# Optimization experiments

Hardware: AMD Instinct MI355X
Metric: run time of the kernel (lower is better)

The kernel has to match this reference:

```python
import jax, jax.numpy as jnp
import numpy as np

T = 4096; D = 768; V = 32000; L = 4; EPS = 1e-5


def _ln(x, g, b):
    m = jnp.mean(x, axis=-1, keepdims=True)
    v = jnp.mean((x - m) ** 2, axis=-1, keepdims=True)
    return (x - m) * jax.lax.rsqrt(v + EPS) * g + b


def _qgelu(x):
    return x * jax.nn.sigmoid(1.702 * x)


def setup_inputs() -> dict:
    key = jax.random.key(0)
    ks = jax.random.split(key, 10)
    s = 0.02
    return {
        "idx": jax.random.randint(ks[0], (T,), 0, V),
        "wte": jax.random.normal(ks[1], (V, D)) * s,
        "rb_ln_g": jnp.ones((D,)), "rb_ln_b": jnp.zeros((D,)),
        "rb_fc_w": jax.random.normal(ks[2], (D, 4 * D)) * s,
        "rb_fc_b": jnp.zeros((4 * D,)),
        "rb_proj_w": jax.random.normal(ks[3], (4 * D, D)) * s,
        "rb_proj_b": jnp.zeros((D,)),
        "lnf_g": jnp.ones((D,)), "lnf_b": jnp.zeros((D,)),
        "lm_head_w": jax.random.normal(ks[4], (D, V)) * s,
        "mb_ln_g": jnp.ones((L, 2 * D)), "mb_ln_b": jnp.zeros((L, 2 * D)),
        "mb_fc_w": jax.random.normal(ks[5], (L, 2 * D, 4 * D)) * s,
        "mb_fc_b": jnp.zeros((L, 4 * D)),
        "mb_proj_w": jax.random.normal(ks[6], (L, 4 * D, D)) * s,
        "mb_proj_b": jnp.zeros((L, D)),
        "op_w": jax.random.normal(ks[7], (L, D, D)) * s,
        "op_b": jnp.zeros((L, D)),
        "lns_g": jnp.ones((L, D)), "lns_b": jnp.zeros((L, D)),
        "heads_w": jax.random.normal(ks[8], (L, D, V)) * s,
    }


def reference(idx, wte, rb_ln_g, rb_ln_b, rb_fc_w, rb_fc_b, rb_proj_w, rb_proj_b,
              lnf_g, lnf_b, lm_head_w, mb_ln_g, mb_ln_b, mb_fc_w, mb_fc_b,
              mb_proj_w, mb_proj_b, op_w, op_b, lns_g, lns_b, heads_w):
    # token embedding (dropout is identity in eval) + initial residual block
    x = wte[idx]  # [T, D]
    h = _ln(x, rb_ln_g, rb_ln_b)
    x = x + _qgelu(h @ rb_fc_w + rb_fc_b) @ rb_proj_w + rb_proj_b
    x = _ln(x, lnf_g, lnf_b)
    logits = x @ lm_head_w  # [T, V]

    # targets=None path: pred_targets = cat(idx[1:], [-1])
    pred_targets = jnp.concatenate([idx[1:], jnp.full((1,), -1, idx.dtype)])
    pos = jnp.arange(T)
    skey = jax.random.key(42)

    for i in range(L):  # static small loop over layers
        j = i + 1
        # multinomial(softmax(logits), 1) == categorical(logits)
        idx_next = jax.random.categorical(jax.random.fold_in(skey, i), logits)
        # positions p where the sample matched the next-token target and p < T - j
        mask = (idx_next == pred_targets) & (pos < T - j)  # [T] bool
        # x2[p] = x[p + j] (padded); compute merge densely, select with mask
        x2 = jnp.concatenate([x[j:], jnp.zeros((j, D), x.dtype)], axis=0)
        h = _ln(jnp.concatenate([x, x2], axis=-1), mb_ln_g[i], mb_ln_b[i])
        merged = x2 + _qgelu(h @ mb_fc_w[i] + mb_fc_b[i]) @ mb_proj_w[i] + mb_proj_b[i]
        # scatter merged[p] into x at position p + j where mask[p]
        merged_s = jnp.concatenate([jnp.zeros((j, D), x.dtype), merged[:-j]], axis=0)
        mask_s = jnp.concatenate([jnp.zeros((j,), bool), mask[:-j]], axis=0)
        x = jnp.where(mask_s[:, None], merged_s, x)
        x = x @ op_w[i] + op_b[i]
        x = _ln(x, lns_g[i], lns_b[i])
        logits = x @ heads_w[i]
    return logits
```

## Files before the change

kernel.cpp:

```cpp
#include <hip/hip_runtime.h>
#include <cstdint>
#include <cstddef>

#define T_TOK 4096
#define DIM   768
#define VOCAB 32000
#define NLAYER 4
#define HALF_TV 65536000u

typedef short bf16x8 __attribute__((ext_vector_type(8)));
typedef float f32x4  __attribute__((ext_vector_type(4)));
typedef float f32x4v __attribute__((ext_vector_type(4)));

__host__ __device__ inline void tf2x32(uint32_t k0, uint32_t k1, uint32_t& v0, uint32_t& v1){
  uint32_t ks2 = k0 ^ k1 ^ 0x1BD11BDAu;
  uint32_t x0 = v0 + k0, x1 = v1 + k1;
#define TFR(R) { x0 += x1; x1 = (x1<<R)|(x1>>(32-R)); x1 ^= x0; }
  TFR(13) TFR(15) TFR(26) TFR(6)
  x0 += k1;  x1 += ks2 + 1u;
  TFR(17) TFR(29) TFR(16) TFR(24)
  x0 += ks2; x1 += k0 + 2u;
  TFR(13) TFR(15) TFR(26) TFR(6)
  x0 += k0;  x1 += k1 + 3u;
  TFR(17) TFR(29) TFR(16) TFR(24)
  x0 += k1;  x1 += ks2 + 4u;
  TFR(13) TFR(15) TFR(26) TFR(6)
  x0 += ks2; x1 += k0 + 5u;
#undef TFR
  v0 = x0; v1 = x1;
}

__device__ inline float neglog_u(uint32_t k){
  float L;
  if (k >= 0x780000u){
    float x = (float)(0x800000u - k) * 1.1920928955078125e-7f;
    L = x * fmaf(x, fmaf(x, fmaf(x, 0.25f, 0.3333333333333f), 0.5f), 1.0f);
  } else {
    float l2k = __builtin_amdgcn_logf((float)k);
    L = 0.69314718055994531f * (23.0f - l2k);
    if (k == 0u) L = 87.33654475055310898f;
  }
  return L;
}

__device__ inline void gumbel_pair(uint32_t kf0, uint32_t kf1, uint32_t t_up, uint32_t v,
                                   float& gu, float& gd){
  uint32_t m = t_up * (uint32_t)VOCAB + v;
  uint32_t x0 = m, x1 = m + HALF_TV;
  tf2x32(kf0, kf1, x0, x1);
  float Lu = neglog_u(x0 >> 9);
  float Ld = neglog_u(x1 >> 9);
  gu = -0.69314718055994531f * __builtin_amdgcn_logf(Lu);
  gd = -0.69314718055994531f * __builtin_amdgcn_logf(Ld);
}

__device__ inline unsigned short f2bf(float f){
  uint32_t u = __float_as_uint(f);
  return (unsigned short)((u + 0x7FFFu + ((u >> 16) & 1u)) >> 16);
}
__device__ inline float bf2f(unsigned short h){
  return __uint_as_float(((uint32_t)h) << 16);
}
__device__ inline void cvt8(const float* f, bool lo, unsigned short* out){
  #pragma unroll
  for (int e=0;e<8;e++){
    float x = f[e];
    unsigned short h = f2bf(x);
    if (lo) h = f2bf(x - bf2f(h));
    out[e] = h;
  }
}
__device__ inline float blockReduceSum(float v){
  __shared__ float red[4];
  #pragma unroll
  for (int off=32; off>0; off>>=1) v += __shfl_down(v, off);
  int w = threadIdx.x >> 6;
  __syncthreads();
  if ((threadIdx.x & 63) == 0) red[w] = v;
  __syncthreads();
  return red[0] + red[1] + red[2] + red[3];
}

__device__ inline void gload16(const void* g, void* l){
  __builtin_amdgcn_global_load_lds(
      (const __attribute__((address_space(1))) unsigned int*)g,
      (__attribute__((address_space(3))) unsigned int*)l, 16, 0, 0);
}

enum { ST_F32 = 0, ST_HILO = 1, ST_SAMPLE = 2 };

template<int KSTEPS, int NSEG, int STORE, bool NTST, bool BIAS, bool QGELU>
__global__ __launch_bounds__(1024, 4) void k_hgemm256(
    const unsigned short* __restrict__ A0, const unsigned short* __restrict__ A1,
    const unsigned short* __restrict__ B0, const unsigned short* __restrict__ B2,
    float* __restrict__ C, unsigned short* __restrict__ Ch, unsigned short* __restrict__ Cl,
    const float* __restrict__ bias, uint32_t kf0, uint32_t kf1,
    unsigned long long* __restrict__ row_best, int N)
{
  constexpr int K  = KSTEPS * 64;
  constexpr int NT = NSEG * KSTEPS;
  __shared__ unsigned short sAll[65536];

  const int t = threadIdx.x;
  const int w = t >> 6, l = t & 63;
  const int wm = w >> 2, wn = w & 3;
  const int g = l >> 4, r = l & 15;

  int bid = blockIdx.x;
  int xcd = bid & 7, c = bid >> 3;
  int bm = xcd*2 + (c & 1);
  int bn = c >> 1;

  f32x4 acc[4][4] = {};

  size_t arow[2], brow[2];
  #pragma unroll
  for (int p=0;p<2;p++){
    int mr = p*128 + (t >> 3);
    int blk = mr >> 4;
    arow[p] = (size_t)(bm*128 + ((blk>>1)<<4) + (mr & 15) + ((blk & 1) ? 2048 : 0)) * K;
    int nr = p*128 + (t >> 3);
    brow[p] = (size_t)(bn*256 + nr) * K;
  }
  const int swz  = ((t & 7) ^ ((t >> 3) & 7)) << 3;
  const int ldst = t * 16;

  auto stage = [&](int vt){
    char* base = (char*)sAll + (vt & 1) * 65536;
    int seg = (NSEG == 1) ? 0 : (vt / KSTEPS);
    int k0  = ((NSEG == 1) ? vt : (vt % KSTEPS)) * 64;
    const unsigned short* Ap = (seg == 1) ? A1 : A0;
    const unsigned short* Bp = (seg == 2) ? B2 : B0;
    #pragma unroll
    for (int p=0;p<2;p++)
      gload16(Ap + arow[p] + k0 + swz, base + p*16384 + ldst);
    #pragma unroll
    for (int p=0;p<2;p++)
      gload16(Bp + brow[p] + k0 + swz, base + 32768 + p*16384 + ldst);
  };

  stage(0);
  __syncthreads();

  for (int vt = 0; vt < NT; ++vt){
    if (vt + 1 < NT) stage(vt + 1);
    const char* sA = (const char*)sAll + (vt & 1) * 65536;
    const char* sB = sA + 32768;
    #pragma unroll
    for (int kk=0;kk<2;kk++){
      bf16x8 bv[4], av[4];
      #pragma unroll
      for (int ni=0;ni<4;ni++){
        int tr = wn*64 + ni*16 + r;
        bv[ni] = *(const bf16x8*)(sB + tr*128 + (((kk*4+g) ^ (r&7))<<4));
      }
      #pragma unroll
      for (int q=0;q<4;q++){
        int tr = wm*64 + q*16 + r;
        av[q] = *(const bf16x8*)(sA + tr*128 + (((kk*4+g) ^ (r&7))<<4));
      }
      __builtin_amdgcn_s_setprio(1);
      #pragma unroll
      for (int q=0;q<4;q++)
        #pragma unroll
        for (int ni=0;ni<4;ni++)
          acc[q][ni] = __builtin_amdgcn_mfma_f32_16x16x32_bf16(av[q], bv[ni], acc[q][ni], 0, 0, 0);
      __builtin_amdgcn_s_setprio(0);
    }
    __syncthreads();
  }

  if constexpr (STORE == ST_SAMPLE){
    #pragma unroll
    for (int mi=0; mi<4; mi+=2){
      int row16 = (wm*2 + (mi>>1)) * 16;
      #pragma unroll
      for (int jj=0;jj<4;jj++){
        uint32_t t_up = bm*128 + row16 + g*4 + jj;
        unsigned long long bu = 0ull, bd = 0ull;
        #pragma unroll
        for (int ni=0;ni<4;ni++){
          uint32_t v = bn*256 + wn*64 + ni*16 + r;
          float gu, gd;
          gumbel_pair(kf0, kf1, t_up, v, gu, gd);
          float vu = acc[mi][ni][jj]   + gu;
          float vd = acc[mi+1][ni][jj] + gd;
          uint32_t fu = __float_as_uint(vu); fu = (fu & 0x80000000u) ? ~fu : (fu | 0x80000000u);
          uint32_t fd = __float_as_uint(vd); fd = (fd & 0x80000000u) ? ~fd : (fd | 0x80000000u);
          unsigned long long pu = ((unsigned long long)fu << 32) | (unsigned long long)(~v);
          unsigned long long pd = ((unsigned long long)fd << 32) | (unsigned long long)(~v);
          if (pu > bu) bu = pu;
          if (pd > bd) bd = pd;
        }
        #pragma unroll
        for (int off=1; off<16; off<<=1){
          unsigned int l0 = (unsigned int)bu, h0 = (unsigned int)(bu>>32);
          unsigned int l1 = __shfl_xor(l0, off), h1 = __shfl_xor(h0, off);
          unsigned long long o = ((unsigned long long)h1 << 32) | (unsigned long long)l1;
          if (o > bu) bu = o;
          l0 = (unsigned int)bd; h0 = (unsigned int)(bd>>32);
          l1 = __shfl_xor(l0, off); h1 = __shfl_xor(h0, off);
          o = ((unsigned long long)h1 << 32) | (unsigned long long)l1;
          if (o > bd) bd = o;
        }
        if (r == 0){
          atomicMax(&row_best[t_up], bu);
          atomicMax(&row_best[t_up + 2048], bd);
        }
      }
    }
  } else {
    #pragma unroll
    for (int mi=0;mi<4;mi++){
      int blk = wm*4 + mi;
      int mbase = bm*128 + ((blk>>1)<<4) + ((blk & 1) ? 2048 : 0);
      #pragma unroll
      for (int ni=0;ni<4;ni++){
        int n = bn*256 + wn*64 + ni*16 + r;
        float bv_ = BIAS ? bias[n] : 0.0f;
        #pragma unroll
        for (int jj=0;jj<4;jj++){
          int m = mbase + g*4 + jj;
          float v = acc[mi][ni][jj] + bv_;
          if constexpr (QGELU) v = v / (1.0f + expf(-1.702f * v));
          if constexpr (STORE == ST_F32){
            if constexpr (NTST) __builtin_nontemporal_store(v, &C[(size_t)m * N + n]);
            else                C[(size_t)m * N + n] = v;
          } else {
            unsigned short h = f2bf(v);
            Ch[(size_t)m * N + n] = h;
            Cl[(size_t)m * N + n] = f2bf(v - bf2f(h));
          }
        }
      }
    }
  }
}

template<int KSTEPS, int NSEG, bool BIAS, bool QGELU, bool RES, int STORE>
__global__ __launch_bounds__(256) void k_hgemm(
    const unsigned short* __restrict__ A0, const unsigned short* __restrict__ A1,
    const unsigned short* __restrict__ B0, const unsigned short* __restrict__ B2,
    float* __restrict__ C, unsigned short* __restrict__ Ch, unsigned short* __restrict__ Cl,
    const float* __restrict__ bias, const float* __restrict__ res,
    int N, uint32_t kf0, uint32_t kf1, unsigned long long* __restrict__ row_best)
{
  constexpr int K = KSTEPS * 64;
  __shared__ unsigned short sA[128*64];
  __shared__ unsigned short sB[128*64];
  const int t = threadIdx.x;
  const int wave = t >> 6, lane = t & 63;
  const int wm = wave >> 1, wn = wave & 1;
  const int g = lane >> 4, r = lane & 15;
  const int lr = lane >> 3, lc = lane & 7;

  int bid = blockIdx.x;
  int xcd = bid & 7, c = bid >> 3;
  int bm = xcd*4 + (c & 3);
  int bn = c >> 2;

  f32x4 acc[4][4] = {};

  for (int kb = 0; kb < NSEG*KSTEPS; ++kb){
    const int seg = (NSEG == 1) ? 0 : (kb / KSTEPS);
    const int k0  = (NSEG == 1) ? kb*64 : (kb % KSTEPS) * 64;
    const unsigned short* Ap = (seg == 1) ? A1 : A0;
    const unsigned short* Bp = (seg == 2) ? B2 : B0;
    __syncthreads();
    #pragma unroll
    for (int p=0;p<4;p++){
      int mr = p*32 + wave*8 + lr;
      int blk = mr >> 4;
      int grow = bm*64 + ((blk>>1)<<4) + (mr & 15) + ((blk & 1) ? 2048 : 0);
      int gk = k0 + ((lc ^ lr) << 3);
      gload16(Ap + (size_t)grow * K + gk, (char*)sA + mr*128 + lc*16);
      int nrow = bn*128 + mr;
      gload16(Bp + (size_t)nrow * K + gk, (char*)sB + mr*128 + lc*16);
    }
    __syncthreads();
    #pragma unroll
    for (int kk=0;kk<2;kk++){
      bf16x8 av[4], bv[4];
      #pragma unroll
      for (int mi=0;mi<4;mi++){
        int tr = wm*64 + mi*16 + r;
        av[mi] = *(const bf16x8*)((const char*)sA + tr*128 + (((kk*4+g) ^ (r&7))<<4));
      }
      #pragma unroll
      for (int ni=0;ni<4;ni++){
        int tr = wn*64 + ni*16 + r;
        bv[ni] = *(const bf16x8*)((const char*)sB + tr*128 + (((kk*4+g) ^ (r&7))<<4));
      }
      #pragma unroll
      for (int mi=0;mi<4;mi++)
        #pragma unroll
        for (int ni=0;ni<4;ni++)
          acc[mi][ni] = __builtin_amdgcn_mfma_f32_16x16x32_bf16(av[mi], bv[ni], acc[mi][ni], 0, 0, 0);
    }
  }

  #pragma unroll
  for (int mi=0;mi<4;mi++){
    int blk2 = wm*4 + mi;
    int mbase = bm*64 + ((blk2>>1)<<4) + ((blk2 & 1) ? 2048 : 0);
    #pragma unroll
    for (int ni=0;ni<4;ni++){
      int n = bn*128 + wn*64 + ni*16 + r;
      float bv_ = BIAS ? bias[n] : 0.0f;
      #pragma unroll
      for (int jj=0;jj<4;jj++){
        int m = mbase + g*4 + jj;
        float v = acc[mi][ni][jj] + bv_;
        if constexpr (QGELU) v = v / (1.0f + expf(-1.702f * v));
        if constexpr (RES)   v += res[(size_t)m * N + n];
        if constexpr (STORE == ST_F32){
          C[(size_t)m * N + n] = v;
        } else {
          unsigned short h = f2bf(v);
          Ch[(size_t)m * N + n] = h;
          Cl[(size_t)m * N + n] = f2bf(v - bf2f(h));
        }
      }
    }
  }
}

template<bool SPLIT>
__global__ __launch_bounds__(256) void k_wt_t(const float* __restrict__ W,
    unsigned short* __restrict__ Bh, unsigned short* __restrict__ Bl, int K, int N)
{
  __shared__ unsigned short sH[64][72];
  __shared__ unsigned short sL[64][72];
  int kt = blockIdx.x, nt = blockIdx.y;
  int t = threadIdx.x;
  int kr = t >> 4, nc4 = (t & 15) * 4;
  #pragma unroll
  for (int p=0;p<4;p++){
    int k = p*16 + kr;
    f32x4v w = __builtin_nontemporal_load((const f32x4v*)&W[(size_t)(kt*64 + k) * N + nt*64 + nc4]);
    #pragma unroll
    for (int e=0;e<4;e++){
      unsigned short h = f2bf(w[e]);
      sH[nc4+e][k] = h;
      if (SPLIT) sL[nc4+e][k] = f2bf(w[e] - bf2f(h));
    }
  }
  __syncthreads();
  #pragma unroll
  for (int q=0;q<2;q++){
    int cid = t + q*256;
    int n = cid >> 3, ch = cid & 7;
    *(bf16x8*)&Bh[(size_t)(nt*64+n)*K + kt*64 + ch*8] = *(const bf16x8*)&sH[n][ch*8];
    if (SPLIT)
      *(bf16x8*)&Bl[(size_t)(nt*64+n)*K + kt*64 + ch*8] = *(const bf16x8*)&sL[n][ch*8];
  }
}

__global__ __launch_bounds__(256) void k_embed_ln(const int* __restrict__ idx,
    const float* __restrict__ wte, const float* __restrict__ g, const float* __restrict__ b,
    float* __restrict__ Xraw, unsigned short* __restrict__ Hh, unsigned short* __restrict__ Hl)
{
  int row = blockIdx.x;
  const float* src = wte + (size_t)idx[row] * DIM;
  float v[3];
  #pragma unroll
  for (int jj=0;jj<3;jj++) v[jj] = src[threadIdx.x + jj*256];
  float s = blockReduceSum(v[0]+v[1]+v[2]);
  float mean = s * (1.0f/DIM);
  float s2 = 0;
  #pragma unroll
  for (int jj=0;jj<3;jj++){ float d = v[jj]-mean; s2 += d*d; }
  s2 = blockReduceSum(s2);
  float rs = rsqrtf(s2 * (1.0f/DIM) + 1e-5f);
  #pragma unroll
  for (int jj=0;jj<3;jj++){
    int d = threadIdx.x + jj*256;
    Xraw[(size_t)row*DIM + d] = v[jj];
    float o = (v[jj]-mean)*rs*g[d] + b[d];
    unsigned short h = f2bf(o);
    Hh[(size_t)row*DIM + d] = h;
    Hl[(size_t)row*DIM + d] = f2bf(o - bf2f(h));
  }
}

__global__ __launch_bounds__(256) void k_ln(const float* __restrict__ in, float* __restrict__ out,
    const float* __restrict__ g, const float* __restrict__ b,
    unsigned short* __restrict__ obf, unsigned short* __restrict__ olo)
{
  int row = blockIdx.x;
  const float* src = in + (size_t)row * DIM;
  float v[3];
  #pragma unroll
  for (int jj=0;jj<3;jj++) v[jj] = src[threadIdx.x + jj*256];
  float s = blockReduceSum(v[0]+v[1]+v[2]);
  float mean = s * (1.0f/DIM);
  float s2 = 0;
  #pragma unroll
  for (int jj=0;jj<3;jj++){ float d = v[jj]-mean; s2 += d*d; }
  s2 = blockReduceSum(s2);
  float rs = rsqrtf(s2 * (1.0f/DIM) + 1e-5f);
  #pragma unroll
  for (int jj=0;jj<3;jj++){
    int d = threadIdx.x + jj*256;
    float o = (v[jj]-mean)*rs*g[d] + b[d];
    out[(size_t)row*DIM + d] = o;
    unsigned short h = f2bf(o);
    obf[(size_t)row*DIM + d] = h;
    olo[(size_t)row*DIM + d] = f2bf(o - bf2f(h));
  }
}

__global__ void k_mask(const unsigned long long* __restrict__ row_best,
    const int* __restrict__ idx, int j, int* __restrict__ count, int* __restrict__ plist)
{
  int t = blockIdx.x * blockDim.x + threadIdx.x;
  if (t >= T_TOK) return;
  int v = (int)(~(uint32_t)(row_best[t] & 0xFFFFFFFFull));
  int tgt = (t < T_TOK-1) ? idx[t+1] : -1;
  if (v == tgt && t < T_TOK - j){
    int pos = atomicAdd(count, 1);
    plist[pos] = t;
  }
}

__global__ __launch_bounds__(256) void k_merge(const float* __restrict__ X,
    const int* __restrict__ plist, const int* __restrict__ count,
    const float* __restrict__ lng, const float* __restrict__ lnb,
    const float* __restrict__ fcw, const float* __restrict__ fcb,
    const float* __restrict__ pjw, const float* __restrict__ pjb,
    float* __restrict__ mergebuf, int j)
{
  __shared__ float sh[1536 + 3072];
  int nb = *count;
  for (int bIdx = blockIdx.x; bIdx < nb; bIdx += gridDim.x){
    int p = plist[bIdx];
    const float* xp = X + (size_t)p * DIM;
    const float* x2 = X + (size_t)(p + j) * DIM;
    for (int d = threadIdx.x; d < 1536; d += 256)
      sh[d] = (d < DIM) ? xp[d] : x2[d - DIM];
    __syncthreads();
    float s = 0;
    for (int d = threadIdx.x; d < 1536; d += 256) s += sh[d];
    s = blockReduceSum(s);
    float mean = s * (1.0f/1536.0f);
    float s2 = 0;
    for (int d = threadIdx.x; d < 1536; d += 256){ float df = sh[d]-mean; s2 += df*df; }
    s2 = blockReduceSum(s2);
    float rs = rsqrtf(s2 * (1.0f/1536.0f) + 1e-5f);
    __syncthreads();
    for (int d = threadIdx.x; d < 1536; d += 256)
      sh[d] = (sh[d]-mean)*rs*lng[d] + lnb[d];
    __syncthreads();
    float* act = sh + 1536;
    #pragma unroll
    for (int jj=0;jj<12;jj++){
      int n = threadIdx.x + jj*256;
      float a = fcb[n];
      for (int k=0;k<1536;k++) a += sh[k]*fcw[(size_t)k*3072 + n];
      act[n] = a / (1.0f + expf(-1.702f*a));
    }
    __syncthreads();
    #pragma unroll
    for (int jj=0;jj<3;jj++){
      int d = threadIdx.x + jj*256;
      float a = pjb[d];
      for (int k=0;k<3072;k++) a += act[k]*pjw[(size_t)k*DIM + d];
      mergebuf[(size_t)bIdx*DIM + d] = x2[d] + a;
    }
    __syncthreads();
  }
}

__global__ void k_scatter(float* __restrict__ X, unsigned short* __restrict__ Xbf,
    unsigned short* __restrict__ Xlo, const float* __restrict__ mergebuf,
    const int* __restrict__ plist, const int* __restrict__ count, int j)
{
  int nb = *count;
  for (int bIdx = blockIdx.x; bIdx < nb; bIdx += gridDim.x){
    int p = plist[bIdx];
    for (int d = threadIdx.x; d < DIM; d += 256){
      float v = mergebuf[(size_t)bIdx*DIM + d];
      size_t o = (size_t)(p + j)*DIM + d;
      X[o] = v;
      unsigned short h = f2bf(v);
      Xbf[o] = h;
      Xlo[o] = f2bf(v - bf2f(h));
    }
  }
}

__global__ __launch_bounds__(256) void k_gemm_old(
    const float* __restrict__ A, const float* __restrict__ B, float* __restrict__ C,
    int M, int N, int K)
{
  __shared__ unsigned short sA[128*64];
  __shared__ unsigned short sB[128*64];
  const int t = threadIdx.x;
  const int bn = blockIdx.x, bm = blockIdx.y;
  const int wave = t >> 6, lane = t & 63;
  const int wm = wave >> 1, wn = wave & 1;
  const int g = lane >> 4, r = lane & 15;
  f32x4 acc[4][4] = {};
  const int nK = K >> 6;
  const int aC = t & 7,  aM0 = t >> 3;
  const int bN0 = t & 31, bC = t >> 5;
  const float* Abase = A + (size_t)(bm*128) * K;
  const float* Bbase = B + (size_t)(bn*128);
  for (int seg = 0; seg < 3; ++seg) {
    const bool aLO = (seg == 1), bLO = (seg == 2);
    for (int kb = 0; kb < nK; ++kb) {
      const int k0 = kb << 6;
      __syncthreads();
      #pragma unroll
      for (int p=0;p<4;p++){
        int m = p*32 + aM0;
        const float* src = Abase + (size_t)m * K + k0 + aC*8;
        float ff[8];
        *(float4*)(ff)   = *(const float4*)(src);
        *(float4*)(ff+4) = *(const float4*)(src+4);
        unsigned short hh[8];
        cvt8(ff, aLO, hh);
        *(bf16x8*)&sA[m*64 + ((aC ^ (m & 7)) * 8)] = *(bf16x8*)hh;
      }
      #pragma unroll
      for (int p=0;p<4;p++){
        int n = p*32 + bN0;
        float ff[8];
        const float* src = Bbase + (size_t)(k0 + bC*8) * N + n;
        #pragma unroll
        for (int e=0;e<8;e++) ff[e] = src[(size_t)e * N];
        unsigned short hh[8];
        cvt8(ff, bLO, hh);
        *(bf16x8*)&sB[n*64 + ((bC ^ (n & 7)) * 8)] = *(bf16x8*)hh;
      }
      __syncthreads();
      #pragma unroll
      for (int kk=0;kk<2;kk++){
        bf16x8 av[4], bv[4];
        #pragma unroll
        for (int mi=0;mi<4;mi++){
          int m = wm*64 + mi*16 + r;
          av[mi] = *(const bf16x8*)&sA[m*64 + (((kk*4 + g) ^ (m & 7)) * 8)];
        }
        #pragma unroll
        for (int ni=0;ni<4;ni++){
          int n = wn*64 + ni*16 + r;
          bv[ni] = *(const bf16x8*)&sB[n*64 + (((kk*4 + g) ^ (n & 7)) * 8)];
        }
        #pragma unroll
        for (int mi=0;mi<4;mi++)
          #pragma unroll
          for (int ni=0;ni<4;ni++)
            acc[mi][ni] = __builtin_amdgcn_mfma_f32_16x16x32_bf16(av[mi], bv[ni], acc[mi][ni], 0, 0, 0);
      }
    }
  }
  #pragma unroll
  for (int mi=0;mi<4;mi++)
    #pragma unroll
    for (int ni=0;ni<4;ni++)
      #pragma unroll
      for (int jj=0;jj<4;jj++){
        int m = bm*128 + wm*64 + mi*16 + g*4 + jj;
        int n = bn*128 + wn*64 + ni*16 + r;
        C[(size_t)m * N + n] = acc[mi][ni][jj];
      }
}

static void fold_key(uint32_t i, uint32_t& o0, uint32_t& o1){
  uint32_t x0 = 0, x1 = i;
  tf2x32(0u, 42u, x0, x1);
  o0 = x0; o1 = x1;
}

extern "C" void kernel_launch(void* const* d_in, const int* in_sizes, int n_in,
                              void* d_out, int out_size, void* d_ws, size_t ws_size,
                              hipStream_t stream)
{
  const int*   idx       = (const int*)  d_in[0];
  const float* wte       = (const float*)d_in[1];
  const float* rb_ln_g   = (const float*)d_in[2];
  const float* rb_ln_b   = (const float*)d_in[3];
  const float* rb_fc_w   = (const float*)d_in[4];
  const float* rb_fc_b   = (const float*)d_in[5];
  const float* rb_proj_w = (const float*)d_in[6];
  const float* rb_proj_b = (const float*)d_in[7];
  const float* lnf_g     = (const float*)d_in[8];
  const float* lnf_b     = (const float*)d_in[9];
  const float* lm_head_w = (const float*)d_in[10];
  const float* mb_ln_g   = (const float*)d_in[11];
  const float* mb_ln_b   = (const float*)d_in[12];
  const float* mb_fc_w   = (const float*)d_in[13];
  const float* mb_fc_b   = (const float*)d_in[14];
  const float* mb_proj_w = (const float*)d_in[15];
  const float* mb_proj_b = (const float*)d_in[16];
  const float* op_w      = (const float*)d_in[17];
  const float* op_b      = (const float*)d_in[18];
  const float* lns_g     = (const float*)d_in[19];
  const float* lns_b     = (const float*)d_in[20];
  const float* heads_w   = (const float*)d_in[21];

  const size_t TD = (size_t)T_TOK * DIM;
  const size_t DV = (size_t)DIM * VOCAB;

  float* X = (float*)d_ws;
  float* Y = X + TD;
  unsigned short* Xbf = (unsigned short*)(Y + TD);
  unsigned short* Xlo = Xbf + TD;
  unsigned short* BtFh = Xlo + TD;
  unsigned short* BtFl = BtFh + DV;
  size_t need_big = (size_t)((char*)(BtFl + DV) - (char*)d_ws);
  bool big = ws_size >= need_big;

  char* ob = (char*)d_out;
  float* OUT = (float*)d_out;
  unsigned short* Hh     = (unsigned short*)(ob);
  unsigned short* Hl     = Hh + TD;
  unsigned short* ACTh   = (unsigned short*)(ob + ((size_t)16<<20));
  unsigned short* ACTl   = ACTh + TD*4;
  unsigned short* Btfc_h = (unsigned short*)(ob + ((size_t)72<<20));
  unsigned short* Btfc_l = Btfc_h + (size_t)3072*DIM;
  unsigned short* Btpj_h = (unsigned short*)(ob + ((size_t)84<<20));
  unsigned short* Btpj_l = Btpj_h + (size_t)3072*DIM;
  unsigned short* BtS    = (unsigned short*)(ob + ((size_t)96<<20));
  unsigned short* Btop_h = (unsigned short*)(ob + ((size_t)152<<20));
  unsigned short* Btop_l = Btop_h + (size_t)DIM*DIM;
  float* MERGE = (float*)(ob + ((size_t)160<<20));
  unsigned long long* ROWBEST = (unsigned long long*)(ob + ((size_t)176<<20));
  int* PLIST = (int*)(ROWBEST + T_TOK);
  int* COUNT = PLIST + T_TOK;

  dim3 blk(256);
  dim3 blk16(1024);

  k_embed_ln<<<T_TOK, blk, 0, stream>>>(idx, wte, rb_ln_g, rb_ln_b, X, Hh, Hl);
  k_wt_t<true><<<dim3(12,48), blk, 0, stream>>>(rb_fc_w,   Btfc_h, Btfc_l, DIM,  3072);
  k_wt_t<true><<<dim3(48,12), blk, 0, stream>>>(rb_proj_w, Btpj_h, Btpj_l, 3072, DIM);
  k_hgemm256<12,3,ST_HILO,false,true,true><<<16*12, blk16, 0, stream>>>(
      Hh, Hl, Btfc_h, Btfc_l, nullptr, ACTh, ACTl, rb_fc_b, 0u,0u, nullptr, 3072);
  k_hgemm<48,3,true,false,true,ST_F32><<<6*32, blk, 0, stream>>>(
      ACTh, ACTl, Btpj_h, Btpj_l, Y, nullptr, nullptr, rb_proj_b, X, DIM, 0u,0u, nullptr);
  k_ln<<<T_TOK, blk, 0, stream>>>(Y, X, lnf_g, lnf_b, Xbf, Xlo);

  for (int i = 0; i < NLAYER; ++i){
    int j = i + 1;
    uint32_t kf0, kf1; fold_key((uint32_t)i, kf0, kf1);

    hipMemsetAsync(ROWBEST, 0, (size_t)T_TOK*8, stream);
    hipMemsetAsync(COUNT, 0, 4, stream);

    const float* hw = (i == 0) ? lm_head_w : heads_w + (size_t)(i-1)*DV;
    k_wt_t<false><<<dim3(12,500), blk, 0, stream>>>(hw, BtS, nullptr, DIM, VOCAB);
    k_hgemm256<12,1,ST_SAMPLE,false,false,false><<<2000, blk16, 0, stream>>>(
        Xbf, Xbf, BtS, BtS, nullptr, nullptr, nullptr, nullptr, kf0, kf1, ROWBEST, VOCAB);

    k_mask<<<T_TOK/256, blk, 0, stream>>>(ROWBEST, idx, j, COUNT, PLIST);
    k_merge<<<64, blk, 0, stream>>>(X, PLIST, COUNT,
        mb_ln_g + (size_t)i*1536, mb_ln_b + (size_t)i*1536,
        mb_fc_w + (size_t)i*1536*3072, mb_fc_b + (size_t)i*3072,
        mb_proj_w + (size_t)i*3072*DIM, mb_proj_b + (size_t)i*DIM, MERGE, j);
    k_scatter<<<64, blk, 0, stream>>>(X, Xbf, Xlo, MERGE, PLIST, COUNT, j);

    k_wt_t<true><<<dim3(12,12), blk, 0, stream>>>(op_w + (size_t)i*DIM*DIM, Btop_h, Btop_l, DIM, DIM);
    k_hgemm<12,3,true,false,false,ST_F32><<<6*32, blk, 0, stream>>>(
        Xbf, Xlo, Btop_h, Btop_l, Y, nullptr, nullptr, op_b + (size_t)i*DIM, nullptr,
        DIM, 0u,0u, nullptr);
    k_ln<<<T_TOK, blk, 0, stream>>>(Y, X, lns_g + (size_t)i*DIM, lns_b + (size_t)i*DIM, Xbf, Xlo);
  }

  if (big){
    k_wt_t<true><<<dim3(12,500), blk, 0, stream>>>(heads_w + (size_t)3*DV, BtFh, BtFl, DIM, VOCAB);
    k_hgemm256<12,3,ST_F32,true,false,false><<<2000, blk16, 0, stream>>>(
        Xbf, Xlo, BtFh, BtFl, OUT, nullptr, nullptr, nullptr, 0u, 0u, nullptr, VOCAB);
  } else {
    k_gemm_old<<<dim3(VOCAB/128, T_TOK/128), blk, 0, stream>>>(
        X, heads_w + (size_t)3*DV, OUT, T_TOK, VOCAB, DIM);
  }
}
```

Before: 2.642 ms.

## Double-buffer LDS tiles in k_hgemm and merge per-layer memsets

Rewrites the small-tile GEMM main loop to use two LDS buffers, so the next K-tile's global loads are issued before the current tile's MFMAs and only one barrier is needed per iteration. Row offsets are precomputed outside the loop. COUNT is moved directly after ROWBEST so a single memset clears both, removing one memset call per layer. Shared memory use doubles to 64KB per block, which may lower occupancy.

```diff
diff --git a/kernel.cpp b/kernel.cpp
--- a/kernel.cpp
+++ b/kernel.cpp
@@ -245,9 +245,10 @@
     const float* __restrict__ bias, const float* __restrict__ res,
     int N, uint32_t kf0, uint32_t kf1, unsigned long long* __restrict__ row_best)
 {
-  constexpr int K = KSTEPS * 64;
-  __shared__ unsigned short sA[128*64];
-  __shared__ unsigned short sB[128*64];
+  constexpr int K  = KSTEPS * 64;
+  constexpr int NT = NSEG * KSTEPS;
+  __shared__ unsigned short sAll[2 * 16 * 1024];
+
   const int t = threadIdx.x;
   const int wave = t >> 6, lane = t & 63;
   const int wm = wave >> 1, wn = wave & 1;
@@ -261,35 +262,49 @@
 
   f32x4 acc[4][4] = {};
 
-  for (int kb = 0; kb < NSEG*KSTEPS; ++kb){
-    const int seg = (NSEG == 1) ? 0 : (kb / KSTEPS);
-    const int k0  = (NSEG == 1) ? kb*64 : (kb % KSTEPS) * 64;
+  size_t arow[4], brow[4];
+  #pragma unroll
+  for (int p=0;p<4;p++){
+    int mr = p*32 + wave*8 + lr;
+    int blk = mr >> 4;
+    arow[p] = (size_t)(bm*64 + ((blk>>1)<<4) + (mr & 15) + ((blk & 1) ? 2048 : 0)) * K;
+    brow[p] = (size_t)(bn*128 + mr) * K;
+  }
+  const int swz  = (lc ^ lr) << 3;
+  const int ldst = (wave*8 + lr)*128 + lc*16;
+
+  auto stage = [&](int vt){
+    char* base = (char*)sAll + (vt & 1) * 32768;
+    int seg = (NSEG == 1) ? 0 : (vt / KSTEPS);
+    int k0  = ((NSEG == 1) ? vt : (vt % KSTEPS)) * 64;
     const unsigned short* Ap = (seg == 1) ? A1 : A0;
     const unsigned short* Bp = (seg == 2) ? B2 : B0;
-    __syncthreads();
     #pragma unroll
     for (int p=0;p<4;p++){
-      int mr = p*32 + wave*8 + lr;
-      int blk = mr >> 4;
-      int grow = bm*64 + ((blk>>1)<<4) + (mr & 15) + ((blk & 1) ? 2048 : 0);
-      int gk = k0 + ((lc ^ lr) << 3);
-      gload16(Ap + (size_t)grow * K + gk, (char*)sA + mr*128 + lc*16);
-      int nrow = bn*128 + mr;
-      gload16(Bp + (size_t)nrow * K + gk, (char*)sB + mr*128 + lc*16);
-    }
-    __syncthreads();
+      gload16(Ap + arow[p] + k0 + swz, base + p*4096 + ldst);
+      gload16(Bp + brow[p] + k0 + swz, base + 16384 + p*4096 + ldst);
+    }
+  };
+
+  stage(0);
+  __syncthreads();
+
+  for (int vt = 0; vt < NT; ++vt){
+    if (vt + 1 < NT) stage(vt + 1);
+    const char* sA = (const char*)sAll + (vt & 1) * 32768;
+    const char* sB = sA + 16384;
     #pragma unroll
     for (int kk=0;kk<2;kk++){
       bf16x8 av[4], bv[4];
       #pragma unroll
       for (int mi=0;mi<4;mi++){
         int tr = wm*64 + mi*16 + r;
-        av[mi] = *(const bf16x8*)((const char*)sA + tr*128 + (((kk*4+g) ^ (r&7))<<4));
+        av[mi] = *(const bf16x8*)(sA + tr*128 + (((kk*4+g) ^ (r&7))<<4));
       }
       #pragma unroll
       for (int ni=0;ni<4;ni++){
         int tr = wn*64 + ni*16 + r;
-        bv[ni] = *(const bf16x8*)((const char*)sB + tr*128 + (((kk*4+g) ^ (r&7))<<4));
+        bv[ni] = *(const bf16x8*)(sB + tr*128 + (((kk*4+g) ^ (r&7))<<4));
       }
       #pragma unroll
       for (int mi=0;mi<4;mi++)
@@ -297,6 +312,7 @@
         for (int ni=0;ni<4;ni++)
           acc[mi][ni] = __builtin_amdgcn_mfma_f32_16x16x32_bf16(av[mi], bv[ni], acc[mi][ni], 0, 0, 0);
     }
+    __syncthreads();
   }
 
   #pragma unroll
@@ -627,8 +643,8 @@
   unsigned short* Btop_l = Btop_h + (size_t)DIM*DIM;
   float* MERGE = (float*)(ob + ((size_t)160<<20));
   unsigned long long* ROWBEST = (unsigned long long*)(ob + ((size_t)176<<20));
-  int* PLIST = (int*)(ROWBEST + T_TOK);
-  int* COUNT = PLIST + T_TOK;
+  int* COUNT = (int*)(ROWBEST + T_TOK);
+  int* PLIST = COUNT + 1;
 
   dim3 blk(256);
   dim3 blk16(1024);
@@ -646,8 +662,7 @@
     int j = i + 1;
     uint32_t kf0, kf1; fold_key((uint32_t)i, kf0, kf1);
 
-    hipMemsetAsync(ROWBEST, 0, (size_t)T_TOK*8, stream);
-    hipMemsetAsync(COUNT, 0, 4, stream);
+    hipMemsetAsync(ROWBEST, 0, (size_t)T_TOK*8 + 4, stream);
 
     const float* hw = (i == 0) ? lm_head_w : heads_w + (size_t)(i-1)*DV;
     k_wt_t<false><<<dim3(12,500), blk, 0, stream>>>(hw, BtS, nullptr, DIM, VOCAB);
```

Measured after the change: 2.564 ms (median of 2 runs). 1.03x faster.
